# Kernel optimization log

Measured on AMD Instinct MI355X. Metric: run time of the kernel, lower is better.

## Reference

```python
import jax, jax.numpy as jnp
import numpy as np

N = 2048      # spatial nodes
K = 4         # blanket size (timesteps)
C = 128       # channels
H = 4         # heads
D = C // H    # head dim
MOD = 256     # mod_features
CTX = 7       # context_features (3+4)
B = 1
TN = N * K


def _make_edges():
    """Faithful numpy port of create_spatio_temporal_edges."""
    rng = np.random.default_rng(0)
    loops = np.stack([np.arange(N), np.arange(N)], axis=1)
    rnd = rng.integers(0, N, size=(N * 15, 2))
    self_edges = np.concatenate([loops, rnd])          # (32768, 2), every node has an edge
    cross_edges = rng.integers(0, N, size=(N * 8, 2))  # (16384, 2)
    spatial = (np.arange(K)[:, None, None] * N + self_edges[None]).reshape(-1, 2)
    temporal = (np.arange(K)[:, None, None] * N + cross_edges[None]).reshape(-1, 2)
    tq, tk = temporal[:, 0], temporal[:, 1]
    E = cross_edges.shape[0]
    parts = [spatial] + [np.stack([tq, np.roll(tk, -(k + 1) * E)], axis=-1) for k in range(K - 1)]
    return np.concatenate(parts).astype(np.int32)   # (327680, 2)


def setup_inputs() -> dict:
    key = jax.random.key(0)
    ks = jax.random.split(key, 16)
    def g(i, shape, scale=0.02):
        return jax.random.normal(ks[i], shape, dtype=jnp.float32) * scale
    return {
        "x": jax.random.normal(ks[0], (B, TN, C), dtype=jnp.float32),
        "time_encoding": jax.random.normal(ks[1], (B, MOD), dtype=jnp.float32),
        "context_encoding": jax.random.normal(ks[2], (B, K, N, CTX), dtype=jnp.float32),
        "edge_index": jnp.asarray(_make_edges()),
        "mod_w1": g(3, (MOD, MOD)), "mod_b1": jnp.zeros((MOD,), jnp.float32),
        "mod_w2": g(4, (3 * C, MOD), 0.0002), "mod_b2": jnp.zeros((3 * C,), jnp.float32),  # last linear scaled by 0.01
        "siren_w0": g(5, (C, CTX), 0.5), "siren_b0": jnp.zeros((C,), jnp.float32),
        "siren_w1": g(6, (C, C)), "siren_b1": jnp.zeros((C,), jnp.float32),
        "wq": g(7, (C, C)), "bq": jnp.zeros((C,), jnp.float32),
        "wk": g(8, (C, C)), "bk": jnp.zeros((C,), jnp.float32),
        "wv": g(9, (C, C)), "bv": jnp.zeros((C,), jnp.float32),
        "wo": g(10, (C, C)), "bo": jnp.zeros((C,), jnp.float32),
        "ffn_w1": g(11, (4 * C, C)), "ffn_b1": jnp.zeros((4 * C,), jnp.float32),
        "ffn_w2": g(12, (C, 4 * C)), "ffn_b2": jnp.zeros((C,), jnp.float32),
    }


def _ln(z, eps=1e-5):
    m = jnp.mean(z, axis=-1, keepdims=True)
    v = jnp.var(z, axis=-1, keepdims=True)
    return (z - m) * jax.lax.rsqrt(v + eps)


def reference(x, time_encoding, context_encoding, edge_index,
              mod_w1, mod_b1, mod_w2, mod_b2,
              siren_w0, siren_b0, siren_w1, siren_b1,
              wq, bq, wk, bk, wv, bv, wo, bo,
              ffn_w1, ffn_b1, ffn_w2, ffn_b2):
    Bx, TNx, Cx = x.shape
    Dh = Cx // H
    # AdaLN modulation: Linear -> SiLU -> Linear -> split into (a, b, c), each (B,1,C)
    t = jax.nn.silu(time_encoding @ mod_w1.T + mod_b1)
    mod = (t @ mod_w2.T + mod_b2).reshape(Bx, 3, Cx)
    a, b, c = mod[:, 0][:, None, :], mod[:, 1][:, None, :], mod[:, 2][:, None, :]
    # SIREN context embedding (1 sin layer + output linear)
    hctx = jnp.sin(context_encoding @ siren_w0.T + siren_b0)
    ctx = (hctx @ siren_w1.T + siren_b1).reshape(Bx, TNx, Cx)
    y = (a + 1.0) * _ln(x + ctx) + b
    # Graph attention over edge list (qk_norm = per-head LayerNorm, no affine)
    q = _ln((y @ wq.T + bq).reshape(Bx, TNx, H, Dh))
    k = _ln((y @ wk.T + bk).reshape(Bx, TNx, H, Dh))
    v = (y @ wv.T + bv).reshape(Bx, TNx, H, Dh)
    src, dst = edge_index[:, 0], edge_index[:, 1]  # query node, key node
    qT = jnp.transpose(q, (1, 0, 2, 3))  # (TN,B,H,D): segment axis first
    kT = jnp.transpose(k, (1, 0, 2, 3))
    vT = jnp.transpose(v, (1, 0, 2, 3))
    qe, ke, ve = qT[src], kT[dst], vT[dst]             # (E,B,H,D)
    s = jnp.einsum('ebhd,ebhd->ebh', qe, ke) / jnp.sqrt(jnp.float32(Dh))
    m = jax.ops.segment_max(s, src, num_segments=TNx)  # (TN,B,H)
    p = jnp.exp(s - m[src])
    denom = jax.ops.segment_sum(p, src, num_segments=TNx)
    agg = jax.ops.segment_sum(p[..., None] * ve, src, num_segments=TNx)  # (TN,B,H,D)
    attn = agg / jnp.maximum(denom, 1e-9)[..., None]
    attn = jnp.transpose(attn, (1, 0, 2, 3)).reshape(Bx, TNx, Cx) @ wo.T + bo
    y = y + attn
    # FFN (no inner residual, matches original)
    y = jax.nn.silu(y @ ffn_w1.T + ffn_b1) @ ffn_w2.T + ffn_b2
    # rsqrt-scaled residual combine
    return (x + c * y) * jax.lax.rsqrt(1.0 + c * c)
```

## Files before the change

kernel.cpp:

```cpp
#include <hip/hip_runtime.h>
#include <math.h>

#define TNODES 8192
#define CC 128
#define RT2 32
#define RT5 32
#define DEGCAP 128

typedef __attribute__((ext_vector_type(8))) short bf8;
typedef __attribute__((ext_vector_type(4))) float fx4;

__device__ __forceinline__ ushort f2b(float f){
  union { float f; uint u; } a; a.f = f;
  uint u = a.u;
  uint r = (u + 0x7fffu + ((u >> 16) & 1u)) >> 16;
  return (ushort)r;
}
__device__ __forceinline__ float b2f(ushort s){
  union { uint u; float f; } a; a.u = ((uint)s) << 16;
  return a.f;
}
__device__ __forceinline__ float2 bpair(uint u){
  union { uint u; float f; } lo, hi;
  lo.u = u << 16; hi.u = u & 0xffff0000u;
  float2 r; r.x = lo.f; r.y = hi.f; return r;
}
#define SWZ(row, col) ((col) ^ (((row) & 7) << 3))

__global__ __launch_bounds__(256) void s1_setup(
    const float* __restrict__ sw1, const float* __restrict__ wq, const float* __restrict__ wk,
    const float* __restrict__ wv, const float* __restrict__ wo, const float* __restrict__ fw1,
    const float* __restrict__ fw2, ushort* __restrict__ dst,
    int* __restrict__ cnt,
    const float* __restrict__ te, const float* __restrict__ mw1, const float* __restrict__ mb1,
    float* __restrict__ tbuf)
{
  const int b = blockIdx.x, tid = threadIdx.x;
  if (b < 208){
    int i = (b * 256 + tid) * 4;
    const float* src; int off;
    if      (i <  16384){ src = sw1; off = i; }
    else if (i <  32768){ src = wq;  off = i - 16384; }
    else if (i <  49152){ src = wk;  off = i - 32768; }
    else if (i <  65536){ src = wv;  off = i - 49152; }
    else if (i <  81920){ src = wo;  off = i - 65536; }
    else if (i < 147456){ src = fw1; off = i - 81920; }
    else                { src = fw2; off = i - 147456; }
    float4 v = *(const float4*)&src[off];
    ushort4 o; o.x = f2b(v.x); o.y = f2b(v.y); o.z = f2b(v.z); o.w = f2b(v.w);
    *(ushort4*)&dst[i] = o;
  } else if (b < 240){
    cnt[(b - 208) * 256 + tid] = 0;
  } else {
    const int og = tid >> 4, th = tid & 15;
    const int o = (b - 240) * 16 + og;
    float acc = 0.f;
    #pragma unroll
    for (int u = 0; u < 4; ++u){
      float4 w  = *(const float4*)&mw1[o*256 + th*16 + u*4];
      float4 t4 = *(const float4*)&te[th*16 + u*4];
      acc += w.x*t4.x + w.y*t4.y + w.z*t4.z + w.w*t4.w;
    }
    #pragma unroll
    for (int m = 1; m < 16; m <<= 1) acc += __shfl_xor(acc, m);
    if (th == 0){
      float z = acc + mb1[o];
      tbuf[o] = z / (1.f + __expf(-z));
    }
  }
}

__global__ __launch_bounds__(512, 4) void k2_ctx_y_qkv(
    const float* __restrict__ x, const float* __restrict__ ce,
    const float* __restrict__ sw0, const float* __restrict__ sb0,
    const ushort* __restrict__ sw1b, const float* __restrict__ sb1,
    const ushort* __restrict__ wqb, const float* __restrict__ bq,
    const ushort* __restrict__ wkb, const float* __restrict__ bk,
    const ushort* __restrict__ wvb, const float* __restrict__ bv,
    const float* __restrict__ tbuf, const float* __restrict__ mw2, const float* __restrict__ mb2,
    ushort* __restrict__ Ybf, ushort* __restrict__ Qb, ushort* __restrict__ Kb, ushort* __restrict__ Vb,
    const int* __restrict__ ei, int E, int* __restrict__ cnt, int* __restrict__ adj)
{
  __shared__ float  ceL[RT2][8];
  __shared__ float  tbL[256];
  __shared__ float  modL[256];
  __shared__ ushort hxb[RT2*CC];
  __shared__ float  yL[RT2][132];
  __shared__ ushort yb[RT2*CC];
  const int tid  = threadIdx.x;

  if (blockIdx.x >= TNODES/RT2){
    const int b = blockIdx.x - TNODES/RT2;
    int e0 = (b * 512 + tid) * 2;
    if (e0 + 1 < E){
      int4 p = *(const int4*)&ei[2*e0];
      int s;
      s = atomicAdd(&cnt[p.x], 1); adj[p.x*DEGCAP + (s & (DEGCAP-1))] = p.y;
      s = atomicAdd(&cnt[p.z], 1); adj[p.z*DEGCAP + (s & (DEGCAP-1))] = p.w;
    } else if (e0 < E){
      int sr = ei[2*e0], ds = ei[2*e0+1];
      int s = atomicAdd(&cnt[sr], 1);
      adj[sr*DEGCAP + (s & (DEGCAP-1))] = ds;
    }
    return;
  }

  const int lane = tid & 63, wave = tid >> 6;
  const int l15 = lane & 15, lg = lane >> 4;
  const int hw  = wave & 3;
  const int rtb = (wave >> 2) * 16;
  const int row0 = blockIdx.x * RT2;

  if (tid < RT2*7){ int r = tid/7, i = tid - r*7; ceL[r][i] = ce[(row0+r)*7 + i]; }
  if (tid < 256) tbL[tid] = tbuf[tid];
  __syncthreads();

  #pragma unroll
  for (int u = 0; u < 8; ++u){
    int idx = tid + u*512;
    int r = idx >> 7, j = idx & 127;
    float a = sb0[j];
    #pragma unroll
    for (int i = 0; i < 7; ++i) a += sw0[j*7+i]*ceL[r][i];
    hxb[r*CC + SWZ(r, j)] = f2b(__sinf(a));
  }

  {
    const int g = tid >> 4, th = tid & 15;
    #pragma unroll
    for (int it = 0; it < 8; ++it){
      int o = g*8 + it;
      float acc = 0.f;
      #pragma unroll
      for (int u = 0; u < 4; ++u){
        float4 wv = *(const float4*)&mw2[o*256 + th*16 + u*4];
        float4 t4 = *(const float4*)&tbL[th*16 + u*4];
        acc += wv.x*t4.x + wv.y*t4.y + wv.z*t4.z + wv.w*t4.w;
      }
      #pragma unroll
      for (int m = 1; m < 16; m <<= 1) acc += __shfl_xor(acc, m);
      if (th == 0) modL[o] = acc + mb2[o];
    }
  }
  __syncthreads();

  const int colb = hw*32;
  {
    bf8 aH[4], bB[8];
    #pragma unroll
    for (int ks = 0; ks < 4; ++ks)
      aH[ks] = *(const bf8*)&hxb[(rtb+l15)*CC + SWZ(rtb+l15, ks*32 + lg*8)];
    #pragma unroll
    for (int ks = 0; ks < 4; ++ks)
      #pragma unroll
      for (int n = 0; n < 2; ++n)
        bB[ks*2+n] = *(const bf8*)&sw1b[(colb + n*16 + l15)*CC + ks*32 + lg*8];
    fx4 acc[2]; acc[0] = 0.f; acc[1] = 0.f;
    #pragma unroll
    for (int ks = 0; ks < 4; ++ks){
      acc[0] = __builtin_amdgcn_mfma_f32_16x16x32_bf16(aH[ks], bB[ks*2+0], acc[0], 0, 0, 0);
      acc[1] = __builtin_amdgcn_mfma_f32_16x16x32_bf16(aH[ks], bB[ks*2+1], acc[1], 0, 0, 0);
    }
    #pragma unroll
    for (int n = 0; n < 2; ++n)
      #pragma unroll
      for (int q = 0; q < 4; ++q){
        int r = rtb + lg*4 + q, c = colb + n*16 + l15;
        yL[r][c] = x[(row0+r)*CC + c] + acc[n][q] + sb1[c];
      }
  }
  __syncthreads();

  {
    int r = tid >> 4, s16 = tid & 15;
    float4 za = *(const float4*)&yL[r][s16*8];
    float4 zb = *(const float4*)&yL[r][s16*8 + 4];
    float sum = za.x+za.y+za.z+za.w + zb.x+zb.y+zb.z+zb.w;
    float ssq = za.x*za.x+za.y*za.y+za.z*za.z+za.w*za.w
              + zb.x*zb.x+zb.y*zb.y+zb.z*zb.z+zb.w*zb.w;
    #pragma unroll
    for (int m = 1; m < 16; m <<= 1){ sum += __shfl_xor(sum, m); ssq += __shfl_xor(ssq, m); }
    float mean = sum * (1.f/128.f);
    float var  = ssq * (1.f/128.f) - mean*mean;
    float inv  = rsqrtf(var + 1e-5f);
    float zv[8] = {za.x,za.y,za.z,za.w,zb.x,zb.y,zb.z,zb.w};
    bf8 pk;
    #pragma unroll
    for (int u = 0; u < 8; ++u){
      int jj = s16*8 + u;
      float z = (zv[u] - mean) * inv;
      pk[u] = (short)f2b((1.f + modL[jj]) * z + modL[128+jj]);
    }
    *(bf8*)&yb[r*CC + SWZ(r, s16*8)] = pk;
  }
  __syncthreads();

  {
    int rr = tid >> 4, b8 = tid & 15;
    bf8 v = *(const bf8*)&yb[rr*CC + SWZ(rr, b8*8)];
    *(bf8*)&Ybf[(row0+rr)*CC + b8*8] = v;
  }

  bf8 af[4];
  #pragma unroll
  for (int ks = 0; ks < 4; ++ks)
    af[ks] = *(const bf8*)&yb[(rtb+l15)*CC + SWZ(rtb+l15, ks*32 + lg*8)];

  const ushort* Wb[3] = {wqb, wkb, wvb};
  const float*  Bs[3] = {bq, bk, bv};
  ushort*       Ob[3] = {Qb, Kb, Vb};
  const int cb = hw*32;
  #pragma unroll
  for (int m = 0; m < 3; ++m){
    bf8 bB[8];
    #pragma unroll
    for (int ks = 0; ks < 4; ++ks)
      #pragma unroll
      for (int n = 0; n < 2; ++n)
        bB[ks*2+n] = *(const bf8*)&Wb[m][(cb + n*16 + l15)*CC + ks*32 + lg*8];
    fx4 acc[2]; acc[0] = 0.f; acc[1] = 0.f;
    #pragma unroll
    for (int ks = 0; ks < 4; ++ks){
      acc[0] = __builtin_amdgcn_mfma_f32_16x16x32_bf16(af[ks], bB[ks*2+0], acc[0], 0, 0, 0);
      acc[1] = __builtin_amdgcn_mfma_f32_16x16x32_bf16(af[ks], bB[ks*2+1], acc[1], 0, 0, 0);
    }
    float vals[2][4];
    #pragma unroll
    for (int n = 0; n < 2; ++n)
      #pragma unroll
      for (int q = 0; q < 4; ++q)
        vals[n][q] = acc[n][q] + Bs[m][cb + n*16 + l15];
    if (m < 2){
      #pragma unroll
      for (int q = 0; q < 4; ++q){
        float s  = vals[0][q] + vals[1][q];
        float ss = vals[0][q]*vals[0][q] + vals[1][q]*vals[1][q];
        #pragma unroll
        for (int mm = 1; mm < 16; mm <<= 1){ s += __shfl_xor(s, mm); ss += __shfl_xor(ss, mm); }
        float mean = s * (1.f/32.f);
        float var  = ss * (1.f/32.f) - mean*mean;
        float inv  = rsqrtf(var + 1e-5f);
        vals[0][q] = (vals[0][q] - mean) * inv;
        vals[1][q] = (vals[1][q] - mean) * inv;
      }
    }
    #pragma unroll
    for (int n = 0; n < 2; ++n)
      #pragma unroll
      for (int q = 0; q < 4; ++q){
        int r = rtb + lg*4 + q, c = cb + n*16 + l15;
        Ob[m][(row0+r)*CC + c] = f2b(vals[n][q]);
      }
  }
}

__global__ __launch_bounds__(512, 2) void k45_attn_ffn(
    const float* __restrict__ x, const ushort* __restrict__ Ybf,
    const ushort* __restrict__ Qb, const ushort* __restrict__ Kb, const ushort* __restrict__ Vb,
    const int* __restrict__ cnt, const int* __restrict__ adj,
    const ushort* __restrict__ wob, const float* __restrict__ bo,
    const ushort* __restrict__ fw1b, const float* __restrict__ fb1,
    const ushort* __restrict__ fw2b, const float* __restrict__ fb2,
    const float* __restrict__ tbuf, const float* __restrict__ mw2, const float* __restrict__ mb2,
    float* __restrict__ out)
{
  __shared__ float  tbL[256];
  __shared__ float  cL[128];
  __shared__ ushort aLb[RT5*CC];
  __shared__ ushort yyb[RT5*CC];
  __shared__ ushort h1b[RT5*512];
  const int tid  = threadIdx.x;
  const int lane = tid & 63, w = tid >> 6;
  const int l15 = lane & 15, lg = lane >> 4;
  const int row0 = blockIdx.x * RT5;

  if (tid < 256) tbL[tid] = tbuf[tid];
  __syncthreads();

  {
    const int g = tid >> 4, th = tid & 15;
    #pragma unroll
    for (int it = 0; it < 4; ++it){
      int o = g*4 + it;
      float acc = 0.f;
      #pragma unroll
      for (int u = 0; u < 4; ++u){
        float4 wv = *(const float4*)&mw2[(256+o)*256 + th*16 + u*4];
        float4 t4 = *(const float4*)&tbL[th*16 + u*4];
        acc += wv.x*t4.x + wv.y*t4.y + wv.z*t4.z + wv.w*t4.w;
      }
      #pragma unroll
      for (int m = 1; m < 16; m <<= 1) acc += __shfl_xor(acc, m);
      if (th == 0) cL[o] = acc + mb2[256+o];
    }
  }

  {
    const int quarter = lane >> 4, ql = lane & 15;
    const int src = row0 + w*4 + quarter;

    uint4 qr = *(const uint4*)&Qb[src*CC + 8*ql];
    float2 qa = bpair(qr.x), qb = bpair(qr.y), qc = bpair(qr.z), qd = bpair(qr.w);
    const float sc = 0.17677669529663687f;
    qa.x*=sc; qa.y*=sc; qb.x*=sc; qb.y*=sc; qc.x*=sc; qc.y*=sc; qd.x*=sc; qd.y*=sc;

    float a0=0.f,a1=0.f,a2=0.f,a3=0.f,a4=0.f,a5=0.f,a6=0.f,a7=0.f, dh=0.f;
    const int deg = min(cnt[src], DEGCAP);
    const int* ab = adj + src*DEGCAP;
    int dmax = deg;
    dmax = max(dmax, __shfl_xor(dmax, 16));
    dmax = max(dmax, __shfl_xor(dmax, 32));

    auto dotk = [&](uint4 kk)->float{
      float2 f0 = bpair(kk.x), f1 = bpair(kk.y), f2 = bpair(kk.z), f3 = bpair(kk.w);
      return qa.x*f0.x+qa.y*f0.y + qb.x*f1.x+qb.y*f1.y + qc.x*f2.x+qc.y*f2.y + qd.x*f3.x+qd.y*f3.y;
    };
    auto accv = [&](uint4 vv, float p){
      float2 f0 = bpair(vv.x), f1 = bpair(vv.y), f2 = bpair(vv.z), f3 = bpair(vv.w);
      a0 += p*f0.x; a1 += p*f0.y; a2 += p*f1.x; a3 += p*f1.y;
      a4 += p*f2.x; a5 += p*f2.y; a6 += p*f3.x; a7 += p*f3.y;
    };

    for (int e = 0; e < dmax; e += 8){
      int4 dA = *(const int4*)&ab[e];
      int4 dB = *(const int4*)&ab[e+4];
      int d0 = (e   < deg) ? dA.x : 0;
      int d1 = (e+1 < deg) ? dA.y : 0;
      int d2 = (e+2 < deg) ? dA.z : 0;
      int d3 = (e+3 < deg) ? dA.w : 0;
      int d4 = (e+4 < deg) ? dB.x : 0;
      int d5 = (e+5 < deg) ? dB.y : 0;
      int d6 = (e+6 < deg) ? dB.z : 0;
      int d7 = (e+7 < deg) ? dB.w : 0;
      uint4 k0 = *(const uint4*)&Kb[d0*CC + 8*ql];
      uint4 k1 = *(const uint4*)&Kb[d1*CC + 8*ql];
      uint4 k2 = *(const uint4*)&Kb[d2*CC + 8*ql];
      uint4 k3 = *(const uint4*)&Kb[d3*CC + 8*ql];
      uint4 k4 = *(const uint4*)&Kb[d4*CC + 8*ql];
      uint4 k5 = *(const uint4*)&Kb[d5*CC + 8*ql];
      uint4 k6 = *(const uint4*)&Kb[d6*CC + 8*ql];
      uint4 k7 = *(const uint4*)&Kb[d7*CC + 8*ql];
      uint4 v0 = *(const uint4*)&Vb[d0*CC + 8*ql];
      uint4 v1 = *(const uint4*)&Vb[d1*CC + 8*ql];
      uint4 v2 = *(const uint4*)&Vb[d2*CC + 8*ql];
      uint4 v3 = *(const uint4*)&Vb[d3*CC + 8*ql];
      uint4 v4 = *(const uint4*)&Vb[d4*CC + 8*ql];
      uint4 v5 = *(const uint4*)&Vb[d5*CC + 8*ql];
      uint4 v6 = *(const uint4*)&Vb[d6*CC + 8*ql];
      uint4 v7 = *(const uint4*)&Vb[d7*CC + 8*ql];

      float p0 = dotk(k0), p1 = dotk(k1), p2 = dotk(k2), p3 = dotk(k3);
      float p4 = dotk(k4), p5 = dotk(k5), p6 = dotk(k6), p7 = dotk(k7);
      p0 += __shfl_xor(p0, 1); p1 += __shfl_xor(p1, 1); p2 += __shfl_xor(p2, 1); p3 += __shfl_xor(p3, 1);
      p4 += __shfl_xor(p4, 1); p5 += __shfl_xor(p5, 1); p6 += __shfl_xor(p6, 1); p7 += __shfl_xor(p7, 1);
      p0 += __shfl_xor(p0, 2); p1 += __shfl_xor(p1, 2); p2 += __shfl_xor(p2, 2); p3 += __shfl_xor(p3, 2);
      p4 += __shfl_xor(p4, 2); p5 += __shfl_xor(p5, 2); p6 += __shfl_xor(p6, 2); p7 += __shfl_xor(p7, 2);
      p0 = (e   < deg) ? __expf(p0) : 0.f;
      p1 = (e+1 < deg) ? __expf(p1) : 0.f;
      p2 = (e+2 < deg) ? __expf(p2) : 0.f;
      p3 = (e+3 < deg) ? __expf(p3) : 0.f;
      p4 = (e+4 < deg) ? __expf(p4) : 0.f;
      p5 = (e+5 < deg) ? __expf(p5) : 0.f;
      p6 = (e+6 < deg) ? __expf(p6) : 0.f;
      p7 = (e+7 < deg) ? __expf(p7) : 0.f;
      accv(v0, p0); accv(v1, p1); accv(v2, p2); accv(v3, p3);
      accv(v4, p4); accv(v5, p5); accv(v6, p6); accv(v7, p7);
      dh += p0 + p1 + p2 + p3 + p4 + p5 + p6 + p7;
    }
    float invd = 1.f / fmaxf(dh, 1e-9f);
    uint4 o4;
    o4.x = (uint)f2b(a0*invd) | ((uint)f2b(a1*invd) << 16);
    o4.y = (uint)f2b(a2*invd) | ((uint)f2b(a3*invd) << 16);
    o4.z = (uint)f2b(a4*invd) | ((uint)f2b(a5*invd) << 16);
    o4.w = (uint)f2b(a6*invd) | ((uint)f2b(a7*invd) << 16);
    int r = w*4 + quarter;
    *(uint4*)&aLb[r*CC + SWZ(r, 8*ql)] = o4;
  }
  __syncthreads();

  {
    const int cw = w*16;
    bf8 aA[2][4], bB[4];
    #pragma unroll
    for (int rt = 0; rt < 2; ++rt)
      #pragma unroll
      for (int ks = 0; ks < 4; ++ks)
        aA[rt][ks] = *(const bf8*)&aLb[(rt*16+l15)*CC + SWZ(rt*16+l15, ks*32 + lg*8)];
    #pragma unroll
    for (int ks = 0; ks < 4; ++ks)
      bB[ks] = *(const bf8*)&wob[(cw + l15)*CC + ks*32 + lg*8];
    fx4 acc[2]; acc[0] = 0.f; acc[1] = 0.f;
    #pragma unroll
    for (int ks = 0; ks < 4; ++ks){
      acc[0] = __builtin_amdgcn_mfma_f32_16x16x32_bf16(aA[0][ks], bB[ks], acc[0], 0, 0, 0);
      acc[1] = __builtin_amdgcn_mfma_f32_16x16x32_bf16(aA[1][ks], bB[ks], acc[1], 0, 0, 0);
    }
    #pragma unroll
    for (int rt = 0; rt < 2; ++rt)
      #pragma unroll
      for (int q = 0; q < 4; ++q){
        int r = rt*16 + lg*4 + q, c = cw + l15;
        float yy = b2f(Ybf[(row0+r)*CC + c]) + acc[rt][q] + bo[c];
        yyb[r*CC + SWZ(r, c)] = f2b(yy);
      }
  }
  __syncthreads();

  {
    const int cb1 = w*64;
    bf8 aY[2][4];
    #pragma unroll
    for (int rt = 0; rt < 2; ++rt)
      #pragma unroll
      for (int ks = 0; ks < 4; ++ks)
        aY[rt][ks] = *(const bf8*)&yyb[(rt*16+l15)*CC + SWZ(rt*16+l15, ks*32 + lg*8)];
    fx4 h[2][4];
    #pragma unroll
    for (int rt = 0; rt < 2; ++rt)
      #pragma unroll
      for (int n = 0; n < 4; ++n) h[rt][n] = 0.f;
    #pragma unroll
    for (int kp = 0; kp < 2; ++kp){
      bf8 bB[8];
      #pragma unroll
      for (int kk = 0; kk < 2; ++kk)
        #pragma unroll
        for (int n = 0; n < 4; ++n)
          bB[kk*4+n] = *(const bf8*)&fw1b[(cb1 + n*16 + l15)*CC + (kp*2+kk)*32 + lg*8];
      #pragma unroll
      for (int kk = 0; kk < 2; ++kk)
        #pragma unroll
        for (int n = 0; n < 4; ++n){
          h[0][n] = __builtin_amdgcn_mfma_f32_16x16x32_bf16(aY[0][kp*2+kk], bB[kk*4+n], h[0][n], 0, 0, 0);
          h[1][n] = __builtin_amdgcn_mfma_f32_16x16x32_bf16(aY[1][kp*2+kk], bB[kk*4+n], h[1][n], 0, 0, 0);
        }
    }
    #pragma unroll
    for (int rt = 0; rt < 2; ++rt)
      #pragma unroll
      for (int n = 0; n < 4; ++n)
        #pragma unroll
        for (int q = 0; q < 4; ++q){
          int r = rt*16 + lg*4 + q, c = cb1 + n*16 + l15;
          float z = h[rt][n][q] + fb1[c];
          float sl = z / (1.f + __expf(-z));
          h1b[r*512 + SWZ(r, c)] = f2b(sl);
        }
  }
  __syncthreads();

  {
    const int cw = w*16;
    fx4 acc[2]; acc[0] = 0.f; acc[1] = 0.f;
    #pragma unroll
    for (int g4 = 0; g4 < 4; ++g4){
      bf8 aH[2][4], bB[4];
      #pragma unroll
      for (int rt = 0; rt < 2; ++rt)
        #pragma unroll
        for (int kk = 0; kk < 4; ++kk)
          aH[rt][kk] = *(const bf8*)&h1b[(rt*16+l15)*512 + SWZ(rt*16+l15, (g4*4+kk)*32 + lg*8)];
      #pragma unroll
      for (int kk = 0; kk < 4; ++kk)
        bB[kk] = *(const bf8*)&fw2b[(cw + l15)*512 + (g4*4+kk)*32 + lg*8];
      #pragma unroll
      for (int kk = 0; kk < 4; ++kk){
        acc[0] = __builtin_amdgcn_mfma_f32_16x16x32_bf16(aH[0][kk], bB[kk], acc[0], 0, 0, 0);
        acc[1] = __builtin_amdgcn_mfma_f32_16x16x32_bf16(aH[1][kk], bB[kk], acc[1], 0, 0, 0);
      }
    }
    #pragma unroll
    for (int rt = 0; rt < 2; ++rt)
      #pragma unroll
      for (int q = 0; q < 4; ++q){
        int r = rt*16 + lg*4 + q, c = cw + l15;
        int g = row0 + r;
        float cj = cL[c];
        float y2 = acc[rt][q] + fb2[c];
        out[g*CC + c] = (x[g*CC + c] + cj*y2) * rsqrtf(1.f + cj*cj);
      }
  }
}

extern "C" void kernel_launch(void* const* d_in, const int* in_sizes, int n_in,
                              void* d_out, int out_size, void* d_ws, size_t ws_size,
                              hipStream_t stream)
{
  const float* x   = (const float*)d_in[0];
  const float* te  = (const float*)d_in[1];
  const float* ce  = (const float*)d_in[2];
  const int*   ei  = (const int*)  d_in[3];
  const float* mw1 = (const float*)d_in[4];
  const float* mb1 = (const float*)d_in[5];
  const float* mw2 = (const float*)d_in[6];
  const float* mb2 = (const float*)d_in[7];
  const float* sw0 = (const float*)d_in[8];
  const float* sb0 = (const float*)d_in[9];
  const float* sw1 = (const float*)d_in[10];
  const float* sb1 = (const float*)d_in[11];
  const float* wq  = (const float*)d_in[12];
  const float* bq  = (const float*)d_in[13];
  const float* wk  = (const float*)d_in[14];
  const float* bk  = (const float*)d_in[15];
  const float* wv  = (const float*)d_in[16];
  const float* bv  = (const float*)d_in[17];
  const float* wo  = (const float*)d_in[18];
  const float* bo  = (const float*)d_in[19];
  const float* fw1 = (const float*)d_in[20];
  const float* fb1 = (const float*)d_in[21];
  const float* fw2 = (const float*)d_in[22];
  const float* fb2 = (const float*)d_in[23];
  float* out = (float*)d_out;
  const int E = in_sizes[3] / 2;

  float* ws   = (float*)d_ws;
  float* tbuf = ws;
  ushort* WB  = (ushort*)(ws + 1024);
  ushort* sw1b = WB;
  ushort* wqb  = WB + 16384;
  ushort* wkb  = WB + 32768;
  ushort* wvb  = WB + 49152;
  ushort* wob  = WB + 65536;
  ushort* fw1b = WB + 81920;
  ushort* fw2b = WB + 147456;
  ushort* Ybf = WB + 212992;
  ushort* Qb  = Ybf + TNODES*CC;
  ushort* Kb  = Qb  + TNODES*CC;
  ushort* Vb  = Kb  + TNODES*CC;
  int* cnt    = (int*)(Vb + TNODES*CC);
  int* adj    = cnt + TNODES;

  const int nSB = (E + 1023) / 1024;

  s1_setup<<<256, 256, 0, stream>>>(sw1, wq, wk, wv, wo, fw1, fw2, WB, cnt, te, mw1, mb1, tbuf);
  k2_ctx_y_qkv<<<TNODES/RT2 + nSB, 512, 0, stream>>>(x, ce, sw0, sb0, sw1b, sb1,
                                              wqb, bq, wkb, bk, wvb, bv,
                                              tbuf, mw2, mb2, Ybf, Qb, Kb, Vb,
                                              ei, E, cnt, adj);
  k45_attn_ffn<<<TNODES/RT5, 512, 0, stream>>>(x, Ybf, Qb, Kb, Vb, cnt, adj,
                                               wob, bo, fw1b, fb1, fw2b, fb2,
                                               tbuf, mw2, mb2, out);
}
```

Measured before the change: 74.80 us.

## Double block size to split edge loop across two wave halves

Launches the attention+FFN kernel with 1024 threads per block. The two halves of the block each process alternate 8-edge chunks of every node's neighbour list, and their partial sums are reduced through shared memory. The MFMA stages are re-tiled so each wave handles one 16-row tile instead of two. The aim is more memory-level parallelism on the gathered K/V loads, which dominate the per-node latency. In exchange it adds an extra reduction and barrier, and the larger block may lower occupancy per CU.

```diff
diff --git a/kernel.cpp b/kernel.cpp
--- a/kernel.cpp
+++ b/kernel.cpp
@@ -254,7 +254,7 @@
   }
 }
 
-__global__ __launch_bounds__(512, 2) void k45_attn_ffn(
+__global__ __launch_bounds__(1024) void k45_attn_ffn(
     const float* __restrict__ x, const ushort* __restrict__ Ybf,
     const ushort* __restrict__ Qb, const ushort* __restrict__ Kb, const ushort* __restrict__ Vb,
     const int* __restrict__ cnt, const int* __restrict__ adj,
@@ -280,8 +280,8 @@
   {
     const int g = tid >> 4, th = tid & 15;
     #pragma unroll
-    for (int it = 0; it < 4; ++it){
-      int o = g*4 + it;
+    for (int it = 0; it < 2; ++it){
+      int o = g*2 + it;
       float acc = 0.f;
       #pragma unroll
       for (int u = 0; u < 4; ++u){
@@ -296,8 +296,11 @@
   }
 
   {
+    const int half = w >> 3;
+    const int sgrp = w & 7;
     const int quarter = lane >> 4, ql = lane & 15;
-    const int src = row0 + w*4 + quarter;
+    const int sl  = sgrp*4 + quarter;
+    const int src = row0 + sl;
 
     uint4 qr = *(const uint4*)&Qb[src*CC + 8*ql];
     float2 qa = bpair(qr.x), qb = bpair(qr.y), qc = bpair(qr.z), qd = bpair(qr.w);
@@ -321,7 +324,7 @@
       a4 += p*f2.x; a5 += p*f2.y; a6 += p*f3.x; a7 += p*f3.y;
     };
 
-    for (int e = 0; e < dmax; e += 8){
+    for (int e = half*8; e < dmax; e += 16){
       int4 dA = *(const int4*)&ab[e];
       int4 dB = *(const int4*)&ab[e+4];
       int d0 = (e   < deg) ? dA.x : 0;
@@ -367,58 +370,63 @@
       accv(v4, p4); accv(v5, p5); accv(v6, p6); accv(v7, p7);
       dh += p0 + p1 + p2 + p3 + p4 + p5 + p6 + p7;
     }
-    float invd = 1.f / fmaxf(dh, 1e-9f);
-    uint4 o4;
-    o4.x = (uint)f2b(a0*invd) | ((uint)f2b(a1*invd) << 16);
-    o4.y = (uint)f2b(a2*invd) | ((uint)f2b(a3*invd) << 16);
-    o4.z = (uint)f2b(a4*invd) | ((uint)f2b(a5*invd) << 16);
-    o4.w = (uint)f2b(a6*invd) | ((uint)f2b(a7*invd) << 16);
-    int r = w*4 + quarter;
-    *(uint4*)&aLb[r*CC + SWZ(r, 8*ql)] = o4;
-  }
-  __syncthreads();
-
-  {
-    const int cw = w*16;
-    bf8 aA[2][4], bB[4];
-    #pragma unroll
-    for (int rt = 0; rt < 2; ++rt)
-      #pragma unroll
-      for (int ks = 0; ks < 4; ++ks)
-        aA[rt][ks] = *(const bf8*)&aLb[(rt*16+l15)*CC + SWZ(rt*16+l15, ks*32 + lg*8)];
+
+    float* pA = (float*)h1b;
+    float* pD = pA + RT5*136;
+    if (half == 1){
+      *(float4*)&pA[sl*136 + 8*ql]     = make_float4(a0, a1, a2, a3);
+      *(float4*)&pA[sl*136 + 8*ql + 4] = make_float4(a4, a5, a6, a7);
+      pD[sl*16 + ql] = dh;
+    }
+    __syncthreads();
+    if (half == 0){
+      float4 u0 = *(const float4*)&pA[sl*136 + 8*ql];
+      float4 u1 = *(const float4*)&pA[sl*136 + 8*ql + 4];
+      a0 += u0.x; a1 += u0.y; a2 += u0.z; a3 += u0.w;
+      a4 += u1.x; a5 += u1.y; a6 += u1.z; a7 += u1.w;
+      dh += pD[sl*16 + ql];
+      float invd = 1.f / fmaxf(dh, 1e-9f);
+      uint4 o4;
+      o4.x = (uint)f2b(a0*invd) | ((uint)f2b(a1*invd) << 16);
+      o4.y = (uint)f2b(a2*invd) | ((uint)f2b(a3*invd) << 16);
+      o4.z = (uint)f2b(a4*invd) | ((uint)f2b(a5*invd) << 16);
+      o4.w = (uint)f2b(a6*invd) | ((uint)f2b(a7*invd) << 16);
+      *(uint4*)&aLb[sl*CC + SWZ(sl, 8*ql)] = o4;
+    }
+  }
+  __syncthreads();
+
+  {
+    const int rw = w >> 3, cw = (w & 7)*16;
+    bf8 aA[4], bB[4];
+    #pragma unroll
+    for (int ks = 0; ks < 4; ++ks)
+      aA[ks] = *(const bf8*)&aLb[(rw*16+l15)*CC + SWZ(rw*16+l15, ks*32 + lg*8)];
     #pragma unroll
     for (int ks = 0; ks < 4; ++ks)
       bB[ks] = *(const bf8*)&wob[(cw + l15)*CC + ks*32 + lg*8];
-    fx4 acc[2]; acc[0] = 0.f; acc[1] = 0.f;
-    #pragma unroll
-    for (int ks = 0; ks < 4; ++ks){
-      acc[0] = __builtin_amdgcn_mfma_f32_16x16x32_bf16(aA[0][ks], bB[ks], acc[0], 0, 0, 0);
-      acc[1] = __builtin_amdgcn_mfma_f32_16x16x32_bf16(aA[1][ks], bB[ks], acc[1], 0, 0, 0);
-    }
-    #pragma unroll
-    for (int rt = 0; rt < 2; ++rt)
-      #pragma unroll
-      for (int q = 0; q < 4; ++q){
-        int r = rt*16 + lg*4 + q, c = cw + l15;
-        float yy = b2f(Ybf[(row0+r)*CC + c]) + acc[rt][q] + bo[c];
-        yyb[r*CC + SWZ(r, c)] = f2b(yy);
-      }
-  }
-  __syncthreads();
-
-  {
-    const int cb1 = w*64;
-    bf8 aY[2][4];
-    #pragma unroll
-    for (int rt = 0; rt < 2; ++rt)
-      #pragma unroll
-      for (int ks = 0; ks < 4; ++ks)
-        aY[rt][ks] = *(const bf8*)&yyb[(rt*16+l15)*CC + SWZ(rt*16+l15, ks*32 + lg*8)];
-    fx4 h[2][4];
-    #pragma unroll
-    for (int rt = 0; rt < 2; ++rt)
-      #pragma unroll
-      for (int n = 0; n < 4; ++n) h[rt][n] = 0.f;
+    fx4 acc; acc = 0.f;
+    #pragma unroll
+    for (int ks = 0; ks < 4; ++ks)
+      acc = __builtin_amdgcn_mfma_f32_16x16x32_bf16(aA[ks], bB[ks], acc, 0, 0, 0);
+    #pragma unroll
+    for (int q = 0; q < 4; ++q){
+      int r = rw*16 + lg*4 + q, c = cw + l15;
+      float yy = b2f(Ybf[(row0+r)*CC + c]) + acc[q] + bo[c];
+      yyb[r*CC + SWZ(r, c)] = f2b(yy);
+    }
+  }
+  __syncthreads();
+
+  {
+    const int rw = w >> 3, cb1 = (w & 7)*64;
+    bf8 aY[4];
+    #pragma unroll
+    for (int ks = 0; ks < 4; ++ks)
+      aY[ks] = *(const bf8*)&yyb[(rw*16+l15)*CC + SWZ(rw*16+l15, ks*32 + lg*8)];
+    fx4 h[4];
+    #pragma unroll
+    for (int n = 0; n < 4; ++n) h[n] = 0.f;
     #pragma unroll
     for (int kp = 0; kp < 2; ++kp){
       bf8 bB[8];
@@ -430,55 +438,45 @@
       #pragma unroll
       for (int kk = 0; kk < 2; ++kk)
         #pragma unroll
-        for (int n = 0; n < 4; ++n){
-          h[0][n] = __builtin_amdgcn_mfma_f32_16x16x32_bf16(aY[0][kp*2+kk], bB[kk*4+n], h[0][n], 0, 0, 0);
-          h[1][n] = __builtin_amdgcn_mfma_f32_16x16x32_bf16(aY[1][kp*2+kk], bB[kk*4+n], h[1][n], 0, 0, 0);
-        }
-    }
-    #pragma unroll
-    for (int rt = 0; rt < 2; ++rt)
-      #pragma unroll
-      for (int n = 0; n < 4; ++n)
-        #pragma unroll
-        for (int q = 0; q < 4; ++q){
-          int r = rt*16 + lg*4 + q, c = cb1 + n*16 + l15;
-          float z = h[rt][n][q] + fb1[c];
-          float sl = z / (1.f + __expf(-z));
-          h1b[r*512 + SWZ(r, c)] = f2b(sl);
-        }
-  }
-  __syncthreads();
-
-  {
-    const int cw = w*16;
-    fx4 acc[2]; acc[0] = 0.f; acc[1] = 0.f;
+        for (int n = 0; n < 4; ++n)
+          h[n] = __builtin_amdgcn_mfma_f32_16x16x32_bf16(aY[kp*2+kk], bB[kk*4+n], h[n], 0, 0, 0);
+    }
+    #pragma unroll
+    for (int n = 0; n < 4; ++n)
+      #pragma unroll
+      for (int q = 0; q < 4; ++q){
+        int r = rw*16 + lg*4 + q, c = cb1 + n*16 + l15;
+        float z = h[n][q] + fb1[c];
+        float sl2 = z / (1.f + __expf(-z));
+        h1b[r*512 + SWZ(r, c)] = f2b(sl2);
+      }
+  }
+  __syncthreads();
+
+  {
+    const int rw = w >> 3, cw = (w & 7)*16;
+    fx4 acc; acc = 0.f;
     #pragma unroll
     for (int g4 = 0; g4 < 4; ++g4){
-      bf8 aH[2][4], bB[4];
-      #pragma unroll
-      for (int rt = 0; rt < 2; ++rt)
-        #pragma unroll
-        for (int kk = 0; kk < 4; ++kk)
-          aH[rt][kk] = *(const bf8*)&h1b[(rt*16+l15)*512 + SWZ(rt*16+l15, (g4*4+kk)*32 + lg*8)];
+      bf8 aH[4], bB[4];
+      #pragma unroll
+      for (int kk = 0; kk < 4; ++kk)
+        aH[kk] = *(const bf8*)&h1b[(rw*16+l15)*512 + SWZ(rw*16+l15, (g4*4+kk)*32 + lg*8)];
       #pragma unroll
       for (int kk = 0; kk < 4; ++kk)
         bB[kk] = *(const bf8*)&fw2b[(cw + l15)*512 + (g4*4+kk)*32 + lg*8];
       #pragma unroll
-      for (int kk = 0; kk < 4; ++kk){
-        acc[0] = __builtin_amdgcn_mfma_f32_16x16x32_bf16(aH[0][kk], bB[kk], acc[0], 0, 0, 0);
-        acc[1] = __builtin_amdgcn_mfma_f32_16x16x32_bf16(aH[1][kk], bB[kk], acc[1], 0, 0, 0);
-      }
-    }
-    #pragma unroll
-    for (int rt = 0; rt < 2; ++rt)
-      #pragma unroll
-      for (int q = 0; q < 4; ++q){
-        int r = rt*16 + lg*4 + q, c = cw + l15;
-        int g = row0 + r;
-        float cj = cL[c];
-        float y2 = acc[rt][q] + fb2[c];
-        out[g*CC + c] = (x[g*CC + c] + cj*y2) * rsqrtf(1.f + cj*cj);
-      }
+      for (int kk = 0; kk < 4; ++kk)
+        acc = __builtin_amdgcn_mfma_f32_16x16x32_bf16(aH[kk], bB[kk], acc, 0, 0, 0);
+    }
+    #pragma unroll
+    for (int q = 0; q < 4; ++q){
+      int r = rw*16 + lg*4 + q, c = cw + l15;
+      int g = row0 + r;
+      float cj = cL[c];
+      float y2 = acc[q] + fb2[c];
+      out[g*CC + c] = (x[g*CC + c] + cj*y2) * rsqrtf(1.f + cj*cj);
+    }
   }
 }
 
@@ -537,7 +535,7 @@
                                               wqb, bq, wkb, bk, wvb, bv,
                                               tbuf, mw2, mb2, Ybf, Qb, Kb, Vb,
                                               ei, E, cnt, adj);
-  k45_attn_ffn<<<TNODES/RT5, 512, 0, stream>>>(x, Ybf, Qb, Kb, Vb, cnt, adj,
-                                               wob, bo, fw1b, fb1, fw2b, fb2,
-                                               tbuf, mw2, mb2, out);
-}
+  k45_attn_ffn<<<TNODES/RT5, 1024, 0, stream>>>(x, Ybf, Qb, Kb, Vb, cnt, adj,
+                                                wob, bo, fw1b, fb1, fw2b, fb2,
+                                                tbuf, mw2, mb2, out);
+}
```

Result: no change. 75.20 us (+0.5%).

## Store K/V in FP8 e4m3 and precompute modulation vector in QKV kernel

Applied to the files above, without the earlier changes.

K and V projections are now written as FP8 e4m3 bytes instead of bf16, halving the gather traffic in the edge-attention loop, and they are decoded with hardware pk conversion builtins when available. The modulation matvec (mw2·t) moves out of every attention block into 12 extra blocks of the QKV kernel, which write it to a workspace buffer. The attention kernel's occupancy hint in launch_bounds is dropped. FP8 storage loses precision on the normalized K and on V, which risks exceeding accuracy tolerance.

```diff
diff --git a/kernel.cpp b/kernel.cpp
--- a/kernel.cpp
+++ b/kernel.cpp
@@ -9,6 +9,7 @@
 
 typedef __attribute__((ext_vector_type(8))) short bf8;
 typedef __attribute__((ext_vector_type(4))) float fx4;
+typedef __attribute__((ext_vector_type(2))) float fv2;
 
 __device__ __forceinline__ ushort f2b(float f){
   union { float f; uint u; } a; a.f = f;
@@ -26,6 +27,60 @@
   float2 r; r.x = lo.f; r.y = hi.f; return r;
 }
 #define SWZ(row, col) ((col) ^ (((row) & 7) << 3))
+
+__device__ __forceinline__ uchar f2e4m3_sw(float f){
+  union { float f; uint u; } a; a.f = f;
+  uint s = a.u >> 31; a.u &= 0x7fffffffu;
+  if (a.f > 448.f) a.f = 448.f;
+  uchar r;
+  if (a.f < 0.0009765625f){ r = 0; }
+  else {
+    uint u = a.u; int ex = (int)(u >> 23) - 127;
+    if (ex < -6){
+      int q = (int)(a.f * 512.f + 0.5f); if (q > 7) q = 7;
+      r = (uchar)q;
+    } else {
+      uint rr = u + 0x7ffffu + ((u >> 20) & 1u);
+      int ex2 = (int)(rr >> 23) - 127;
+      uint m3 = (rr >> 20) & 7u;
+      int eb = ex2 + 7;
+      if (eb > 15 || (eb == 15 && m3 > 6)){ eb = 15; m3 = 6; }
+      r = (uchar)((eb << 3) | m3);
+    }
+  }
+  return (uchar)(r | (s << 7));
+}
+__device__ __forceinline__ float e4m3f_sw(uchar b){
+  uint s = b >> 7, e = (b >> 3) & 15u, m = b & 7u;
+  float v;
+  if (e == 0) v = (float)m * 0.001953125f;
+  else { union { uint u; float f; } t; t.u = ((e + 120u) << 23) | (m << 20); v = t.f; }
+  return s ? -v : v;
+}
+#if __has_builtin(__builtin_amdgcn_cvt_pk_fp8_f32)
+__device__ __forceinline__ uchar f2e4m3(float f){
+  uint t = (uint)__builtin_amdgcn_cvt_pk_fp8_f32(f, 0.f, 0, false);
+  return (uchar)(t & 0xffu);
+}
+#else
+__device__ __forceinline__ uchar f2e4m3(float f){ return f2e4m3_sw(f); }
+#endif
+#if __has_builtin(__builtin_amdgcn_cvt_pk_f32_fp8)
+template<bool WORD>
+__device__ __forceinline__ float2 e8pair(uint u){
+  fv2 r = __builtin_amdgcn_cvt_pk_f32_fp8(u, WORD);
+  float2 o; o.x = r.x; o.y = r.y; return o;
+}
+#else
+template<bool WORD>
+__device__ __forceinline__ float2 e8pair(uint u){
+  uint sh = WORD ? 16u : 0u;
+  float2 o;
+  o.x = e4m3f_sw((uchar)((u >> sh) & 0xffu));
+  o.y = e4m3f_sw((uchar)((u >> (sh + 8u)) & 0xffu));
+  return o;
+}
+#endif
 
 __global__ __launch_bounds__(256) void s1_setup(
     const float* __restrict__ sw1, const float* __restrict__ wq, const float* __restrict__ wk,
@@ -78,7 +133,9 @@
     const ushort* __restrict__ wkb, const float* __restrict__ bk,
     const ushort* __restrict__ wvb, const float* __restrict__ bv,
     const float* __restrict__ tbuf, const float* __restrict__ mw2, const float* __restrict__ mb2,
-    ushort* __restrict__ Ybf, ushort* __restrict__ Qb, ushort* __restrict__ Kb, ushort* __restrict__ Vb,
+    float* __restrict__ mod,
+    ushort* __restrict__ Ybf, ushort* __restrict__ Qb,
+    uchar* __restrict__ Kb8, uchar* __restrict__ Vb8,
     const int* __restrict__ ei, int E, int* __restrict__ cnt, int* __restrict__ adj)
 {
   __shared__ float  ceL[RT2][8];
@@ -90,17 +147,33 @@
   const int tid  = threadIdx.x;
 
   if (blockIdx.x >= TNODES/RT2){
-    const int b = blockIdx.x - TNODES/RT2;
-    int e0 = (b * 512 + tid) * 2;
-    if (e0 + 1 < E){
-      int4 p = *(const int4*)&ei[2*e0];
-      int s;
-      s = atomicAdd(&cnt[p.x], 1); adj[p.x*DEGCAP + (s & (DEGCAP-1))] = p.y;
-      s = atomicAdd(&cnt[p.z], 1); adj[p.z*DEGCAP + (s & (DEGCAP-1))] = p.w;
-    } else if (e0 < E){
-      int sr = ei[2*e0], ds = ei[2*e0+1];
-      int s = atomicAdd(&cnt[sr], 1);
-      adj[sr*DEGCAP + (s & (DEGCAP-1))] = ds;
+    const int b2 = blockIdx.x - TNODES/RT2;
+    if (b2 < (int)((E + 1023) / 1024)){
+      int e0 = (b2 * 512 + tid) * 2;
+      if (e0 + 1 < E){
+        int4 p = *(const int4*)&ei[2*e0];
+        int s;
+        s = atomicAdd(&cnt[p.x], 1); adj[p.x*DEGCAP + (s & (DEGCAP-1))] = p.y;
+        s = atomicAdd(&cnt[p.z], 1); adj[p.z*DEGCAP + (s & (DEGCAP-1))] = p.w;
+      } else if (e0 < E){
+        int sr = ei[2*e0], ds = ei[2*e0+1];
+        int s = atomicAdd(&cnt[sr], 1);
+        adj[sr*DEGCAP + (s & (DEGCAP-1))] = ds;
+      }
+    } else {
+      const int mb = b2 - (int)((E + 1023) / 1024);
+      const int og = tid >> 4, th = tid & 15;
+      const int o = mb*32 + og;
+      float acc = 0.f;
+      #pragma unroll
+      for (int u = 0; u < 4; ++u){
+        float4 wv = *(const float4*)&mw2[o*256 + th*16 + u*4];
+        float4 t4 = *(const float4*)&tbuf[th*16 + u*4];
+        acc += wv.x*t4.x + wv.y*t4.y + wv.z*t4.z + wv.w*t4.w;
+      }
+      #pragma unroll
+      for (int m = 1; m < 16; m <<= 1) acc += __shfl_xor(acc, m);
+      if (th == 0) mod[o] = acc + mb2[o];
     }
     return;
   }
@@ -208,7 +281,6 @@
 
   const ushort* Wb[3] = {wqb, wkb, wvb};
   const float*  Bs[3] = {bq, bk, bv};
-  ushort*       Ob[3] = {Qb, Kb, Vb};
   const int cb = hw*32;
   #pragma unroll
   for (int m = 0; m < 3; ++m){
@@ -249,22 +321,22 @@
       #pragma unroll
       for (int q = 0; q < 4; ++q){
         int r = rtb + lg*4 + q, c = cb + n*16 + l15;
-        Ob[m][(row0+r)*CC + c] = f2b(vals[n][q]);
-      }
-  }
-}
-
-__global__ __launch_bounds__(512, 2) void k45_attn_ffn(
+        if (m == 0)      Qb [(row0+r)*CC + c] = f2b(vals[n][q]);
+        else if (m == 1) Kb8[(row0+r)*CC + c] = f2e4m3(vals[n][q]);
+        else             Vb8[(row0+r)*CC + c] = f2e4m3(vals[n][q]);
+      }
+  }
+}
+
+__global__ __launch_bounds__(512) void k45_attn_ffn(
     const float* __restrict__ x, const ushort* __restrict__ Ybf,
-    const ushort* __restrict__ Qb, const ushort* __restrict__ Kb, const ushort* __restrict__ Vb,
+    const ushort* __restrict__ Qb, const uchar* __restrict__ Kb8, const uchar* __restrict__ Vb8,
     const int* __restrict__ cnt, const int* __restrict__ adj,
     const ushort* __restrict__ wob, const float* __restrict__ bo,
     const ushort* __restrict__ fw1b, const float* __restrict__ fb1,
     const ushort* __restrict__ fw2b, const float* __restrict__ fb2,
-    const float* __restrict__ tbuf, const float* __restrict__ mw2, const float* __restrict__ mb2,
-    float* __restrict__ out)
+    const float* __restrict__ mod, float* __restrict__ out)
 {
-  __shared__ float  tbL[256];
   __shared__ float  cL[128];
   __shared__ ushort aLb[RT5*CC];
   __shared__ ushort yyb[RT5*CC];
@@ -274,26 +346,8 @@
   const int l15 = lane & 15, lg = lane >> 4;
   const int row0 = blockIdx.x * RT5;
 
-  if (tid < 256) tbL[tid] = tbuf[tid];
-  __syncthreads();
-
-  {
-    const int g = tid >> 4, th = tid & 15;
-    #pragma unroll
-    for (int it = 0; it < 4; ++it){
-      int o = g*4 + it;
-      float acc = 0.f;
-      #pragma unroll
-      for (int u = 0; u < 4; ++u){
-        float4 wv = *(const float4*)&mw2[(256+o)*256 + th*16 + u*4];
-        float4 t4 = *(const float4*)&tbL[th*16 + u*4];
-        acc += wv.x*t4.x + wv.y*t4.y + wv.z*t4.z + wv.w*t4.w;
-      }
-      #pragma unroll
-      for (int m = 1; m < 16; m <<= 1) acc += __shfl_xor(acc, m);
-      if (th == 0) cL[o] = acc + mb2[256+o];
-    }
-  }
+  if (tid < 128) cL[tid] = mod[256 + tid];
+  __syncthreads();
 
   {
     const int quarter = lane >> 4, ql = lane & 15;
@@ -311,14 +365,16 @@
     dmax = max(dmax, __shfl_xor(dmax, 16));
     dmax = max(dmax, __shfl_xor(dmax, 32));
 
-    auto dotk = [&](uint4 kk)->float{
-      float2 f0 = bpair(kk.x), f1 = bpair(kk.y), f2 = bpair(kk.z), f3 = bpair(kk.w);
-      return qa.x*f0.x+qa.y*f0.y + qb.x*f1.x+qb.y*f1.y + qc.x*f2.x+qc.y*f2.y + qd.x*f3.x+qd.y*f3.y;
+    auto dotk = [&](uint2 kk)->float{
+      float2 e0 = e8pair<false>(kk.x), e1 = e8pair<true>(kk.x);
+      float2 e2 = e8pair<false>(kk.y), e3 = e8pair<true>(kk.y);
+      return qa.x*e0.x+qa.y*e0.y + qb.x*e1.x+qb.y*e1.y + qc.x*e2.x+qc.y*e2.y + qd.x*e3.x+qd.y*e3.y;
     };
-    auto accv = [&](uint4 vv, float p){
-      float2 f0 = bpair(vv.x), f1 = bpair(vv.y), f2 = bpair(vv.z), f3 = bpair(vv.w);
-      a0 += p*f0.x; a1 += p*f0.y; a2 += p*f1.x; a3 += p*f1.y;
-      a4 += p*f2.x; a5 += p*f2.y; a6 += p*f3.x; a7 += p*f3.y;
+    auto accv = [&](uint2 vv, float p){
+      float2 e0 = e8pair<false>(vv.x), e1 = e8pair<true>(vv.x);
+      float2 e2 = e8pair<false>(vv.y), e3 = e8pair<true>(vv.y);
+      a0 += p*e0.x; a1 += p*e0.y; a2 += p*e1.x; a3 += p*e1.y;
+      a4 += p*e2.x; a5 += p*e2.y; a6 += p*e3.x; a7 += p*e3.y;
     };
 
     for (int e = 0; e < dmax; e += 8){
@@ -332,22 +388,22 @@
       int d5 = (e+5 < deg) ? dB.y : 0;
       int d6 = (e+6 < deg) ? dB.z : 0;
       int d7 = (e+7 < deg) ? dB.w : 0;
-      uint4 k0 = *(const uint4*)&Kb[d0*CC + 8*ql];
-      uint4 k1 = *(const uint4*)&Kb[d1*CC + 8*ql];
-      uint4 k2 = *(const uint4*)&Kb[d2*CC + 8*ql];
-      uint4 k3 = *(const uint4*)&Kb[d3*CC + 8*ql];
-      uint4 k4 = *(const uint4*)&Kb[d4*CC + 8*ql];
-      uint4 k5 = *(const uint4*)&Kb[d5*CC + 8*ql];
-      uint4 k6 = *(const uint4*)&Kb[d6*CC + 8*ql];
-      uint4 k7 = *(const uint4*)&Kb[d7*CC + 8*ql];
-      uint4 v0 = *(const uint4*)&Vb[d0*CC + 8*ql];
-      uint4 v1 = *(const uint4*)&Vb[d1*CC + 8*ql];
-      uint4 v2 = *(const uint4*)&Vb[d2*CC + 8*ql];
-      uint4 v3 = *(const uint4*)&Vb[d3*CC + 8*ql];
-      uint4 v4 = *(const uint4*)&Vb[d4*CC + 8*ql];
-      uint4 v5 = *(const uint4*)&Vb[d5*CC + 8*ql];
-      uint4 v6 = *(const uint4*)&Vb[d6*CC + 8*ql];
-      uint4 v7 = *(const uint4*)&Vb[d7*CC + 8*ql];
+      uint2 k0 = *(const uint2*)&Kb8[d0*CC + 8*ql];
+      uint2 k1 = *(const uint2*)&Kb8[d1*CC + 8*ql];
+      uint2 k2 = *(const uint2*)&Kb8[d2*CC + 8*ql];
+      uint2 k3 = *(const uint2*)&Kb8[d3*CC + 8*ql];
+      uint2 k4 = *(const uint2*)&Kb8[d4*CC + 8*ql];
+      uint2 k5 = *(const uint2*)&Kb8[d5*CC + 8*ql];
+      uint2 k6 = *(const uint2*)&Kb8[d6*CC + 8*ql];
+      uint2 k7 = *(const uint2*)&Kb8[d7*CC + 8*ql];
+      uint2 v0 = *(const uint2*)&Vb8[d0*CC + 8*ql];
+      uint2 v1 = *(const uint2*)&Vb8[d1*CC + 8*ql];
+      uint2 v2 = *(const uint2*)&Vb8[d2*CC + 8*ql];
+      uint2 v3 = *(const uint2*)&Vb8[d3*CC + 8*ql];
+      uint2 v4 = *(const uint2*)&Vb8[d4*CC + 8*ql];
+      uint2 v5 = *(const uint2*)&Vb8[d5*CC + 8*ql];
+      uint2 v6 = *(const uint2*)&Vb8[d6*CC + 8*ql];
+      uint2 v7 = *(const uint2*)&Vb8[d7*CC + 8*ql];
 
       float p0 = dotk(k0), p1 = dotk(k1), p2 = dotk(k2), p3 = dotk(k3);
       float p4 = dotk(k4), p5 = dotk(k5), p6 = dotk(k6), p7 = dotk(k7);
@@ -515,6 +571,7 @@
 
   float* ws   = (float*)d_ws;
   float* tbuf = ws;
+  float* mod  = ws + 512;
   ushort* WB  = (ushort*)(ws + 1024);
   ushort* sw1b = WB;
   ushort* wqb  = WB + 16384;
@@ -525,19 +582,19 @@
   ushort* fw2b = WB + 147456;
   ushort* Ybf = WB + 212992;
   ushort* Qb  = Ybf + TNODES*CC;
-  ushort* Kb  = Qb  + TNODES*CC;
-  ushort* Vb  = Kb  + TNODES*CC;
-  int* cnt    = (int*)(Vb + TNODES*CC);
+  uchar*  Kb8 = (uchar*)(Qb + TNODES*CC);
+  uchar*  Vb8 = Kb8 + TNODES*CC;
+  int* cnt    = (int*)(Vb8 + TNODES*CC);
   int* adj    = cnt + TNODES;
 
   const int nSB = (E + 1023) / 1024;
 
   s1_setup<<<256, 256, 0, stream>>>(sw1, wq, wk, wv, wo, fw1, fw2, WB, cnt, te, mw1, mb1, tbuf);
-  k2_ctx_y_qkv<<<TNODES/RT2 + nSB, 512, 0, stream>>>(x, ce, sw0, sb0, sw1b, sb1,
+  k2_ctx_y_qkv<<<TNODES/RT2 + nSB + 12, 512, 0, stream>>>(x, ce, sw0, sb0, sw1b, sb1,
                                               wqb, bq, wkb, bk, wvb, bv,
-                                              tbuf, mw2, mb2, Ybf, Qb, Kb, Vb,
+                                              tbuf, mw2, mb2, mod, Ybf, Qb, Kb8, Vb8,
                                               ei, E, cnt, adj);
-  k45_attn_ffn<<<TNODES/RT5, 512, 0, stream>>>(x, Ybf, Qb, Kb, Vb, cnt, adj,
+  k45_attn_ffn<<<TNODES/RT5, 512, 0, stream>>>(x, Ybf, Qb, Kb8, Vb8, cnt, adj,
                                                wob, bo, fw1b, fb1, fw2b, fb2,
-                                               tbuf, mw2, mb2, out);
-}
+                                               mod, out);
+}
```

Result: faster. 69.82 us (-6.7%).
